# Optimization experiments

Hardware: AMD Instinct MI355X
Metric: run time of the kernel (lower is better)

## Reference

```python
import jax, jax.numpy as jnp
import numpy as np

N_NODES = 100000
IN_DIM = 128
HID_DIM = 128
N_EDGES = 1600000


def setup_inputs() -> dict:
    key = jax.random.key(0)
    k1, k2, k3, k4 = jax.random.split(key, 4)
    x = jax.random.normal(k1, (N_NODES, IN_DIM), dtype=jnp.float32)
    edge_index = jax.random.randint(k2, (2, N_EDGES), 0, N_NODES, dtype=jnp.int64)
    # GCNConv params (PyG: Linear(in, out, bias=False) + separate bias)
    scale = 1.0 / np.sqrt(IN_DIM)
    weight = jax.random.uniform(k3, (IN_DIM, HID_DIM), jnp.float32, -scale, scale)
    bias = jax.random.uniform(k4, (HID_DIM,), jnp.float32, -scale, scale)
    return {"x": x, "edge_index": edge_index, "weight": weight, "bias": bias}


def _gcn_forward(x, edge_index, weight, bias):
    n = x.shape[0]
    h = x @ weight  # [N, H] linear transform first (PyG order)
    # add self-loops
    loops = jnp.arange(n, dtype=edge_index.dtype)
    src = jnp.concatenate([edge_index[0], loops])
    dst = jnp.concatenate([edge_index[1], loops])
    # symmetric normalization: deg computed on destination (col) per PyG gcn_norm
    ones = jnp.ones_like(dst, dtype=h.dtype)
    deg = jax.ops.segment_sum(ones, dst, num_segments=n)  # [N]
    dinv = jnp.where(deg > 0, jax.lax.rsqrt(deg), 0.0)
    norm = dinv[src] * dinv[dst]  # [E+N]
    # message passing: out[dst] += norm * h[src]
    msg = h[src] * norm[:, None]  # [E+N, H] irregular gather (memory-bound)
    out = jax.ops.segment_sum(msg, dst, num_segments=n)  # scatter-add
    return out + bias


def reference(x, edge_index, weight, bias):
    h = _gcn_forward(x, edge_index, weight, bias)
    return jax.nn.relu(h)  # encoder_type != 'gat' -> ReLU
```

## Files before the change

### kernel.cpp

```cpp
#include <hip/hip_runtime.h>
#include <hip/hip_bf16.h>

#define N_NODES 100000
#define IN_DIM 128
#define HID_DIM 128
#define N_EDGES 1600000
#define NBK 196
#define BCAP 10240
#define BK_EDGES 4096
#define NBIN 391
#define NGEMM 1563
#define G1 625
#define G2 (NGEMM - G1)
#define LDK 136

using half8 = __attribute__((ext_vector_type(8))) _Float16;
using half4 = __attribute__((ext_vector_type(4))) _Float16;
using f32x4 = __attribute__((ext_vector_type(4))) float;

__global__ void k_prep(int* __restrict__ gcur, const float* __restrict__ w,
                       _Float16* __restrict__ wt) {
    int i = blockIdx.x * 256 + threadIdx.x;
    if (i < NBK) gcur[i] = 0;
    if (i < IN_DIM * HID_DIM) {
        int k = i >> 7, c = i & 127;
        wt[c * 128 + k] = (_Float16)w[i];
    }
}

__device__ __forceinline__ void gemm_role(char* smem, int tid, int brow,
                                          const float* __restrict__ x,
                                          const _Float16* __restrict__ wt,
                                          _Float16* __restrict__ h) {
    _Float16* xs = (_Float16*)smem;
    _Float16* ws = (_Float16*)(smem + 17408);
    {
        int row = tid >> 2;
        int seg = (tid & 3) * 32;
        int grow = brow + row; if (grow > N_NODES - 1) grow = N_NODES - 1;
        const float4* p = reinterpret_cast<const float4*>(&x[(size_t)grow * IN_DIM + seg]);
#pragma unroll
        for (int i = 0; i < 8; ++i) {
            float4 v = p[i];
            half4 hv = {(_Float16)v.x, (_Float16)v.y, (_Float16)v.z, (_Float16)v.w};
            *reinterpret_cast<half4*>(&xs[row * LDK + seg + i * 4]) = hv;
        }
    }
    {
        int row = tid >> 1;
        int seg = (tid & 1) * 64;
        const half8* p = reinterpret_cast<const half8*>(&wt[row * 128 + seg]);
#pragma unroll
        for (int i = 0; i < 8; ++i)
            *reinterpret_cast<half8*>(&ws[row * LDK + seg + i * 8]) = p[i];
    }
    __syncthreads();

    const int lane = tid & 63;
    const int m0   = (tid >> 6) * 16;
    const int arow = m0 + (lane & 15);
    const int kgrp = (lane >> 4) * 8;
    f32x4 acc[8] = {};
#pragma unroll
    for (int k0 = 0; k0 < 128; k0 += 32) {
        half8 a = *reinterpret_cast<const half8*>(&xs[arow * LDK + k0 + kgrp]);
#pragma unroll
        for (int nb = 0; nb < 8; ++nb) {
            half8 b = *reinterpret_cast<const half8*>(
                &ws[(nb * 16 + (lane & 15)) * LDK + k0 + kgrp]);
            acc[nb] = __builtin_amdgcn_mfma_f32_16x16x32_f16(a, b, acc[nb], 0, 0, 0);
        }
    }
#pragma unroll
    for (int nb = 0; nb < 8; ++nb) {
#pragma unroll
        for (int r = 0; r < 4; ++r) {
            int node = brow + m0 + (lane >> 4) * 4 + r;
            int feat = nb * 16 + (lane & 15);
            if (node < N_NODES) h[(size_t)node * HID_DIM + feat] = (_Float16)acc[nb][r];
        }
    }
}

__global__ __launch_bounds__(256) void k_fat1(const int* __restrict__ ei,
                                              const float* __restrict__ x,
                                              const _Float16* __restrict__ wt,
                                              _Float16* __restrict__ h,
                                              int* __restrict__ gcur,
                                              uint2* __restrict__ bucket) {
    __shared__ __align__(16) char smem[52224];
    const int tid = threadIdx.x;

    if (blockIdx.x >= NBIN) {
        gemm_role(smem, tid, (blockIdx.x - NBIN) * 64, x, wt, h);
        return;
    }
    uint2* stage = (uint2*)smem;
    int* hist  = (int*)(smem + 32768);
    int* lbase = (int*)(smem + 33552);
    int* lcur  = (int*)(smem + 34336);
    int* s64   = (int*)(smem + 35120);
    for (int b = tid; b < NBK; b += 256) { hist[b] = 0; lcur[b] = 0; }
    if (tid < 64) {
        int v = ei[2 * tid + 1];
        int all0 = __all(v == 0);
        if (tid == 0) *s64 = all0;
    }
    __syncthreads();
    const int is64 = *s64;
    const int e0 = blockIdx.x * BK_EDGES;
    const int valid = min(BK_EDGES, N_EDGES - e0);

#pragma unroll
    for (int k = 0; k < 8; ++k) {
        int el = k * 512 + 2 * tid;
        if (el >= valid) break;
        int e = e0 + el;
        int s0, s1, d0, d1;
        if (is64) {
            int4 vs = reinterpret_cast<const int4*>(ei)[e >> 1];
            int4 vd = (reinterpret_cast<const int4*>(ei) + N_EDGES / 2)[e >> 1];
            s0 = vs.x; s1 = vs.z; d0 = vd.x; d1 = vd.z;
        } else {
            int2 vs = reinterpret_cast<const int2*>(ei)[e >> 1];
            int2 vd = reinterpret_cast<const int2*>(ei + N_EDGES)[e >> 1];
            s0 = vs.x; s1 = vs.y; d0 = vd.x; d1 = vd.y;
        }
        stage[el]     = make_uint2((unsigned)s0, (unsigned)d0);
        stage[el + 1] = make_uint2((unsigned)s1, (unsigned)d1);
        atomicAdd(&hist[d0 >> 9], 1);
        atomicAdd(&hist[d1 >> 9], 1);
    }
    __syncthreads();
    for (int b = tid; b < NBK; b += 256)
        if (hist[b] > 0) lbase[b] = atomicAdd(&gcur[b], hist[b]);
    __syncthreads();
    for (int i = tid; i < valid; i += 256) {
        uint2 v = stage[i];
        int b = v.y >> 9;
        int pos = lbase[b] + atomicAdd(&lcur[b], 1);
        if (pos < BCAP) bucket[(size_t)b * BCAP + pos] = v;
    }
}

__global__ __launch_bounds__(256) void k_fat2(const int* __restrict__ gcur,
                                              const uint2* __restrict__ bucket,
                                              int* __restrict__ cnt,
                                              float* __restrict__ dinv,
                                              int* __restrict__ row_start,
                                              int* __restrict__ csr_src,
                                              const float* __restrict__ x,
                                              const _Float16* __restrict__ wt,
                                              _Float16* __restrict__ h) {
    __shared__ __align__(16) char smem[52224];
    const int tid = threadIdx.x;

    if (blockIdx.x >= NBK) {
        gemm_role(smem, tid, (G1 + blockIdx.x - NBK) * 64, x, wt, h);
        return;
    }
    int* sizes = (int*)smem;
    int* ncnt  = (int*)(smem + 784);
    int* nloff = (int*)(smem + 2832);
    int* ncur  = (int*)(smem + 4880);
    int* wtot  = (int*)(smem + 6928);
    int* base_p = (int*)(smem + 6944);
    const int b = blockIdx.x;
    for (int i = tid; i < NBK; i += 256) sizes[i] = gcur[i];
    ncnt[tid] = 0; ncnt[tid + 256] = 0; ncur[tid] = 0; ncur[tid + 256] = 0;
    __syncthreads();
    const int sz = min(sizes[b], BCAP);
    if (tid < 64) {
        int part = 0;
        for (int i = tid; i < b; i += 64) part += sizes[i];
#pragma unroll
        for (int d = 32; d; d >>= 1) part += __shfl_xor(part, d);
        if (tid == 0) *base_p = part;
    }
    const int n0 = b * 512;
    const uint2* bk = bucket + (size_t)b * BCAP;
    for (int i = tid; i < sz; i += 256) atomicAdd(&ncnt[bk[i].y - n0], 1);
    __syncthreads();
    int c0 = ncnt[2 * tid], c1 = ncnt[2 * tid + 1];
    int pair = c0 + c1;
    int lane = tid & 63, wv = tid >> 6;
    int scan = pair;
#pragma unroll
    for (int d = 1; d < 64; d <<= 1) {
        int t = __shfl_up(scan, d);
        if (lane >= d) scan += t;
    }
    if (lane == 63) wtot[wv] = scan;
    int excl = scan - pair;
    __syncthreads();
#pragma unroll
    for (int i = 0; i < 4; ++i) if (i < wv) excl += wtot[i];
    nloff[2 * tid] = excl;
    nloff[2 * tid + 1] = excl + c0;
    __syncthreads();
    const int base = *base_p;
    for (int i = tid; i < 512; i += 256) {
        int node = n0 + i;
        if (node < N_NODES) {
            int c = ncnt[i];
            cnt[node] = c;
            dinv[node] = rsqrtf((float)(c + 1));
            row_start[node] = base + nloff[i];
        }
    }
    for (int i = tid; i < sz; i += 256) {
        uint2 v = bk[i];
        int li = v.y - n0;
        int pos = atomicAdd(&ncur[li], 1);
        csr_src[base + nloff[li] + pos] = (int)v.x;
    }
}

#define GSTEP(J, SE, DS) {                                                   \
    int s_ = __shfl(SE, hi | (J));                                           \
    float w_ = __shfl(DS, hi | (J));                                         \
    half8 v_ = *reinterpret_cast<const half8*>(hbase + (size_t)s_ * HID_DIM);\
    acc[0] = fmaf((float)v_[0], w_, acc[0]);                                 \
    acc[1] = fmaf((float)v_[1], w_, acc[1]);                                 \
    acc[2] = fmaf((float)v_[2], w_, acc[2]);                                 \
    acc[3] = fmaf((float)v_[3], w_, acc[3]);                                 \
    acc[4] = fmaf((float)v_[4], w_, acc[4]);                                 \
    acc[5] = fmaf((float)v_[5], w_, acc[5]);                                 \
    acc[6] = fmaf((float)v_[6], w_, acc[6]);                                 \
    acc[7] = fmaf((float)v_[7], w_, acc[7]); }
#define GGRP(B, SE, DS) \
    GSTEP(B + 0, SE, DS) GSTEP(B + 1, SE, DS) GSTEP(B + 2, SE, DS) \
    GSTEP(B + 3, SE, DS) GSTEP(B + 4, SE, DS) GSTEP(B + 5, SE, DS) \
    GSTEP(B + 6, SE, DS) GSTEP(B + 7, SE, DS)

__global__ __launch_bounds__(256) void k_gather(const _Float16* __restrict__ h,
                                                const int* __restrict__ csr_src,
                                                const int* __restrict__ row_start,
                                                const int* __restrict__ cnt,
                                                const float* __restrict__ dinv,
                                                const float* __restrict__ bias,
                                                float* __restrict__ out) {
    const int lane = threadIdx.x & 63;
    const int l4   = lane & 15;
    const int hi   = lane & 48;
    const int node = blockIdx.x * 16 + (threadIdx.x >> 6) * 4 + (lane >> 4);
    const int rs = row_start[node];
    const int n  = cnt[node];
    const float di = dinv[node];
    const int tq = n + 1;
    const _Float16* hbase = h + l4 * 8;

    float acc[8] = {};

    for (int c0 = 0; c0 < tq; c0 += 32) {
        int t0 = c0 + l4, t1 = t0 + 16;
        int se0 = node, se1 = node;
        float dw0 = 0.0f, dw1 = 0.0f;
        if (t0 < n)       { se0 = csr_src[rs + t0]; dw0 = dinv[se0]; }
        else if (t0 == n)   dw0 = di;
        if (t1 < n)       { se1 = csr_src[rs + t1]; dw1 = dinv[se1]; }
        else if (t1 == n)   dw1 = di;

        GGRP(0, se0, dw0)
        if (tq <= c0 + 8) continue;
        GGRP(8, se0, dw0)
        if (tq <= c0 + 16) continue;
        GGRP(0, se1, dw1)
        if (tq <= c0 + 24) continue;
        GGRP(8, se1, dw1)
    }

    float4 bv0 = *reinterpret_cast<const float4*>(&bias[l4 * 8]);
    float4 bv1 = *reinterpret_cast<const float4*>(&bias[l4 * 8 + 4]);
    float4 o0, o1;
    o0.x = fmaxf(fmaf(di, acc[0], bv0.x), 0.0f);
    o0.y = fmaxf(fmaf(di, acc[1], bv0.y), 0.0f);
    o0.z = fmaxf(fmaf(di, acc[2], bv0.z), 0.0f);
    o0.w = fmaxf(fmaf(di, acc[3], bv0.w), 0.0f);
    o1.x = fmaxf(fmaf(di, acc[4], bv1.x), 0.0f);
    o1.y = fmaxf(fmaf(di, acc[5], bv1.y), 0.0f);
    o1.z = fmaxf(fmaf(di, acc[6], bv1.z), 0.0f);
    o1.w = fmaxf(fmaf(di, acc[7], bv1.w), 0.0f);
    *reinterpret_cast<float4*>(&out[(size_t)node * HID_DIM + l4 * 8])     = o0;
    *reinterpret_cast<float4*>(&out[(size_t)node * HID_DIM + l4 * 8 + 4]) = o1;
}

extern "C" void kernel_launch(void* const* d_in, const int* in_sizes, int n_in,
                              void* d_out, int out_size, void* d_ws, size_t ws_size,
                              hipStream_t stream) {
    const float* x    = (const float*)d_in[0];
    const int*   ei   = (const int*)d_in[1];
    const float* w    = (const float*)d_in[2];
    const float* bias = (const float*)d_in[3];
    float* out = (float*)d_out;

    char* wsb = (char*)d_ws;
    _Float16* h      = (_Float16*)(wsb);
    int*   cnt       = (int*)(wsb + 25600000);
    float* dinv      = (float*)(wsb + 26000000);
    int*   row_start = (int*)(wsb + 26400000);
    int*   csr_src   = (int*)(wsb + 26800000);
    uint2* bucket    = (uint2*)(wsb + 33200000);
    _Float16* wt     = (_Float16*)(wsb + 49256320);
    int*   gcur      = (int*)(wsb + 49289088);

    k_prep  <<<64, 256, 0, stream>>>(gcur, w, wt);
    k_fat1  <<<NBIN + G1, 256, 0, stream>>>(ei, x, wt, h, gcur, bucket);
    k_fat2  <<<NBK + G2, 256, 0, stream>>>(gcur, bucket, cnt, dinv, row_start, csr_src, x, wt, h);
    k_gather<<<N_NODES / 16, 256, 0, stream>>>(h, csr_src, row_start, cnt, dinv, bias, out);
}
```

Measured before the change: 123.3 us.

## Slice h by feature groups and gather per slice for cache locality

The GEMM now writes h in a feature-sliced layout: 8 slices of 16 features for all nodes. The gather kernel is restructured so each block handles one slice for a chunk of 128 nodes, with 2 lanes per node each accumulating 8 features over a sequential edge loop. The aim is to make each slice's working set small enough to stay in L2 during the random gathers. In exchange, edge indices and dinv are reread once per slice, each gather access is smaller, and per-lane loops serialize over node degree.

```diff
diff --git a/kernel.cpp b/kernel.cpp
--- a/kernel.cpp
+++ b/kernel.cpp
@@ -13,6 +13,9 @@
 #define G1 625
 #define G2 (NGEMM - G1)
 #define LDK 136
+#define SLICE_ELEMS (N_NODES * 16)
+#define GCHUNK 128
+#define NCHUNK ((N_NODES + GCHUNK - 1) / GCHUNK)
 
 using half8 = __attribute__((ext_vector_type(8))) _Float16;
 using half4 = __attribute__((ext_vector_type(4))) _Float16;
@@ -76,8 +79,9 @@
 #pragma unroll
         for (int r = 0; r < 4; ++r) {
             int node = brow + m0 + (lane >> 4) * 4 + r;
-            int feat = nb * 16 + (lane & 15);
-            if (node < N_NODES) h[(size_t)node * HID_DIM + feat] = (_Float16)acc[nb][r];
+            if (node < N_NODES)
+                h[(size_t)nb * SLICE_ELEMS + (size_t)node * 16 + (lane & 15)] =
+                    (_Float16)acc[nb][r];
         }
     }
 }
@@ -216,23 +220,6 @@
     }
 }
 
-#define GSTEP(J, SE, DS) {                                                   \
-    int s_ = __shfl(SE, hi | (J));                                           \
-    float w_ = __shfl(DS, hi | (J));                                         \
-    half8 v_ = *reinterpret_cast<const half8*>(hbase + (size_t)s_ * HID_DIM);\
-    acc[0] = fmaf((float)v_[0], w_, acc[0]);                                 \
-    acc[1] = fmaf((float)v_[1], w_, acc[1]);                                 \
-    acc[2] = fmaf((float)v_[2], w_, acc[2]);                                 \
-    acc[3] = fmaf((float)v_[3], w_, acc[3]);                                 \
-    acc[4] = fmaf((float)v_[4], w_, acc[4]);                                 \
-    acc[5] = fmaf((float)v_[5], w_, acc[5]);                                 \
-    acc[6] = fmaf((float)v_[6], w_, acc[6]);                                 \
-    acc[7] = fmaf((float)v_[7], w_, acc[7]); }
-#define GGRP(B, SE, DS) \
-    GSTEP(B + 0, SE, DS) GSTEP(B + 1, SE, DS) GSTEP(B + 2, SE, DS) \
-    GSTEP(B + 3, SE, DS) GSTEP(B + 4, SE, DS) GSTEP(B + 5, SE, DS) \
-    GSTEP(B + 6, SE, DS) GSTEP(B + 7, SE, DS)
-
 __global__ __launch_bounds__(256) void k_gather(const _Float16* __restrict__ h,
                                                 const int* __restrict__ csr_src,
                                                 const int* __restrict__ row_start,
@@ -240,49 +227,59 @@
                                                 const float* __restrict__ dinv,
                                                 const float* __restrict__ bias,
                                                 float* __restrict__ out) {
-    const int lane = threadIdx.x & 63;
-    const int l4   = lane & 15;
-    const int hi   = lane & 48;
-    const int node = blockIdx.x * 16 + (threadIdx.x >> 6) * 4 + (lane >> 4);
-    const int rs = row_start[node];
-    const int n  = cnt[node];
-    const float di = dinv[node];
-    const int tq = n + 1;
-    const _Float16* hbase = h + l4 * 8;
-
-    float acc[8] = {};
-
-    for (int c0 = 0; c0 < tq; c0 += 32) {
-        int t0 = c0 + l4, t1 = t0 + 16;
-        int se0 = node, se1 = node;
-        float dw0 = 0.0f, dw1 = 0.0f;
-        if (t0 < n)       { se0 = csr_src[rs + t0]; dw0 = dinv[se0]; }
-        else if (t0 == n)   dw0 = di;
-        if (t1 < n)       { se1 = csr_src[rs + t1]; dw1 = dinv[se1]; }
-        else if (t1 == n)   dw1 = di;
-
-        GGRP(0, se0, dw0)
-        if (tq <= c0 + 8) continue;
-        GGRP(8, se0, dw0)
-        if (tq <= c0 + 16) continue;
-        GGRP(0, se1, dw1)
-        if (tq <= c0 + 24) continue;
-        GGRP(8, se1, dw1)
-    }
-
-    float4 bv0 = *reinterpret_cast<const float4*>(&bias[l4 * 8]);
-    float4 bv1 = *reinterpret_cast<const float4*>(&bias[l4 * 8 + 4]);
-    float4 o0, o1;
-    o0.x = fmaxf(fmaf(di, acc[0], bv0.x), 0.0f);
-    o0.y = fmaxf(fmaf(di, acc[1], bv0.y), 0.0f);
-    o0.z = fmaxf(fmaf(di, acc[2], bv0.z), 0.0f);
-    o0.w = fmaxf(fmaf(di, acc[3], bv0.w), 0.0f);
-    o1.x = fmaxf(fmaf(di, acc[4], bv1.x), 0.0f);
-    o1.y = fmaxf(fmaf(di, acc[5], bv1.y), 0.0f);
-    o1.z = fmaxf(fmaf(di, acc[6], bv1.z), 0.0f);
-    o1.w = fmaxf(fmaf(di, acc[7], bv1.w), 0.0f);
-    *reinterpret_cast<float4*>(&out[(size_t)node * HID_DIM + l4 * 8])     = o0;
-    *reinterpret_cast<float4*>(&out[(size_t)node * HID_DIM + l4 * 8 + 4]) = o1;
+    const int slice = blockIdx.x & 7;
+    const int chunk = blockIdx.x >> 3;
+    const int lane  = threadIdx.x & 63;
+    const int oct   = lane & 1;
+    const int node  = chunk * GCHUNK + (threadIdx.x >> 6) * 32 + (lane >> 1);
+    const bool ok = node < N_NODES;
+    const int nd  = ok ? node : N_NODES - 1;
+    const int rs  = row_start[nd];
+    const int n   = ok ? cnt[nd] : 0;
+    const float di = dinv[nd];
+    const _Float16* hS = h + (size_t)slice * SLICE_ELEMS + oct * 8;
+
+    float acc[8];
+    {
+        half8 v = *reinterpret_cast<const half8*>(hS + (size_t)nd * 16);
+#pragma unroll
+        for (int k = 0; k < 8; ++k) acc[k] = di * (float)v[k];
+    }
+    int j = 0;
+    for (; j + 2 <= n; j += 2) {
+        int s0 = csr_src[rs + j], s1 = csr_src[rs + j + 1];
+        float w0 = dinv[s0], w1 = dinv[s1];
+        half8 v0 = *reinterpret_cast<const half8*>(hS + (size_t)s0 * 16);
+        half8 v1 = *reinterpret_cast<const half8*>(hS + (size_t)s1 * 16);
+#pragma unroll
+        for (int k = 0; k < 8; ++k) acc[k] = fmaf((float)v0[k], w0, acc[k]);
+#pragma unroll
+        for (int k = 0; k < 8; ++k) acc[k] = fmaf((float)v1[k], w1, acc[k]);
+    }
+    if (j < n) {
+        int s0 = csr_src[rs + j];
+        float w0 = dinv[s0];
+        half8 v0 = *reinterpret_cast<const half8*>(hS + (size_t)s0 * 16);
+#pragma unroll
+        for (int k = 0; k < 8; ++k) acc[k] = fmaf((float)v0[k], w0, acc[k]);
+    }
+    if (ok) {
+        const int fb = slice * 16 + oct * 8;
+        float4 bv0 = *reinterpret_cast<const float4*>(&bias[fb]);
+        float4 bv1 = *reinterpret_cast<const float4*>(&bias[fb + 4]);
+        float4 o0, o1;
+        o0.x = fmaxf(fmaf(di, acc[0], bv0.x), 0.0f);
+        o0.y = fmaxf(fmaf(di, acc[1], bv0.y), 0.0f);
+        o0.z = fmaxf(fmaf(di, acc[2], bv0.z), 0.0f);
+        o0.w = fmaxf(fmaf(di, acc[3], bv0.w), 0.0f);
+        o1.x = fmaxf(fmaf(di, acc[4], bv1.x), 0.0f);
+        o1.y = fmaxf(fmaf(di, acc[5], bv1.y), 0.0f);
+        o1.z = fmaxf(fmaf(di, acc[6], bv1.z), 0.0f);
+        o1.w = fmaxf(fmaf(di, acc[7], bv1.w), 0.0f);
+        float* op = &out[(size_t)node * HID_DIM + fb];
+        *reinterpret_cast<float4*>(op)     = o0;
+        *reinterpret_cast<float4*>(op + 4) = o1;
+    }
 }
 
 extern "C" void kernel_launch(void* const* d_in, const int* in_sizes, int n_in,
@@ -307,5 +304,5 @@
     k_prep  <<<64, 256, 0, stream>>>(gcur, w, wt);
     k_fat1  <<<NBIN + G1, 256, 0, stream>>>(ei, x, wt, h, gcur, bucket);
     k_fat2  <<<NBK + G2, 256, 0, stream>>>(gcur, bucket, cnt, dinv, row_start, csr_src, x, wt, h);
-    k_gather<<<N_NODES / 16, 256, 0, stream>>>(h, csr_src, row_start, cnt, dinv, bias, out);
-}
+    k_gather<<<NCHUNK * 8, 256, 0, stream>>>(h, csr_src, row_start, cnt, dinv, bias, out);
+}
```

New measurement: 219.4 us. 77.9% more time.

## Pack bucket entries into 32-bit words and merge row_start/count arrays

Applied to the files above, without the earlier changes.

Bucket entries are now stored as one 32-bit word (source shifted left by 9, plus the local destination index), with the bucket id kept separately in shared memory. This halves bucket write and read traffic and shrinks shared staging. k_fat2 holds up to 40 entries per thread in registers so the bucket is read once instead of twice. row_start and cnt are merged into one int2 array so the gather kernel does a single load per node. The costs are higher register pressure in k_fat2 and reliance on source ids fitting in 23 bits.

```diff
diff --git a/kernel.cpp b/kernel.cpp
--- a/kernel.cpp
+++ b/kernel.cpp
@@ -87,7 +87,7 @@
                                               const _Float16* __restrict__ wt,
                                               _Float16* __restrict__ h,
                                               int* __restrict__ gcur,
-                                              uint2* __restrict__ bucket) {
+                                              unsigned* __restrict__ bucket) {
     __shared__ __align__(16) char smem[52224];
     const int tid = threadIdx.x;
 
@@ -95,11 +95,12 @@
         gemm_role(smem, tid, (blockIdx.x - NBIN) * 64, x, wt, h);
         return;
     }
-    uint2* stage = (uint2*)smem;
-    int* hist  = (int*)(smem + 32768);
-    int* lbase = (int*)(smem + 33552);
-    int* lcur  = (int*)(smem + 34336);
-    int* s64   = (int*)(smem + 35120);
+    unsigned* stage = (unsigned*)smem;
+    unsigned char* bkid = (unsigned char*)(smem + 16384);
+    int* hist  = (int*)(smem + 20480);
+    int* lbase = (int*)(smem + 21264);
+    int* lcur  = (int*)(smem + 22048);
+    int* s64   = (int*)(smem + 22832);
     for (int b = tid; b < NBK; b += 256) { hist[b] = 0; lcur[b] = 0; }
     if (tid < 64) {
         int v = ei[2 * tid + 1];
@@ -126,8 +127,10 @@
             int2 vd = reinterpret_cast<const int2*>(ei + N_EDGES)[e >> 1];
             s0 = vs.x; s1 = vs.y; d0 = vd.x; d1 = vd.y;
         }
-        stage[el]     = make_uint2((unsigned)s0, (unsigned)d0);
-        stage[el + 1] = make_uint2((unsigned)s1, (unsigned)d1);
+        stage[el]     = ((unsigned)s0 << 9) | ((unsigned)d0 & 511u);
+        stage[el + 1] = ((unsigned)s1 << 9) | ((unsigned)d1 & 511u);
+        bkid[el]      = (unsigned char)(d0 >> 9);
+        bkid[el + 1]  = (unsigned char)(d1 >> 9);
         atomicAdd(&hist[d0 >> 9], 1);
         atomicAdd(&hist[d1 >> 9], 1);
     }
@@ -136,18 +139,17 @@
         if (hist[b] > 0) lbase[b] = atomicAdd(&gcur[b], hist[b]);
     __syncthreads();
     for (int i = tid; i < valid; i += 256) {
-        uint2 v = stage[i];
-        int b = v.y >> 9;
+        unsigned v = stage[i];
+        int b = bkid[i];
         int pos = lbase[b] + atomicAdd(&lcur[b], 1);
         if (pos < BCAP) bucket[(size_t)b * BCAP + pos] = v;
     }
 }
 
 __global__ __launch_bounds__(256) void k_fat2(const int* __restrict__ gcur,
-                                              const uint2* __restrict__ bucket,
-                                              int* __restrict__ cnt,
+                                              const unsigned* __restrict__ bucket,
                                               float* __restrict__ dinv,
-                                              int* __restrict__ row_start,
+                                              int2* __restrict__ rc,
                                               int* __restrict__ csr_src,
                                               const float* __restrict__ x,
                                               const _Float16* __restrict__ wt,
@@ -178,8 +180,15 @@
         if (tid == 0) *base_p = part;
     }
     const int n0 = b * 512;
-    const uint2* bk = bucket + (size_t)b * BCAP;
-    for (int i = tid; i < sz; i += 256) atomicAdd(&ncnt[bk[i].y - n0], 1);
+    const unsigned* bk = bucket + (size_t)b * BCAP;
+    unsigned ent[40];
+#pragma unroll
+    for (int j = 0; j < 40; ++j) {
+        int i = j * 256 + tid;
+        unsigned v = 0xFFFFFFFFu;
+        if (i < sz) { v = bk[i]; atomicAdd(&ncnt[v & 511u], 1); }
+        ent[j] = v;
+    }
     __syncthreads();
     int c0 = ncnt[2 * tid], c1 = ncnt[2 * tid + 1];
     int pair = c0 + c1;
@@ -203,16 +212,18 @@
         int node = n0 + i;
         if (node < N_NODES) {
             int c = ncnt[i];
-            cnt[node] = c;
             dinv[node] = rsqrtf((float)(c + 1));
-            row_start[node] = base + nloff[i];
-        }
-    }
-    for (int i = tid; i < sz; i += 256) {
-        uint2 v = bk[i];
-        int li = v.y - n0;
-        int pos = atomicAdd(&ncur[li], 1);
-        csr_src[base + nloff[li] + pos] = (int)v.x;
+            rc[node] = make_int2(base + nloff[i], c);
+        }
+    }
+#pragma unroll
+    for (int j = 0; j < 40; ++j) {
+        unsigned v = ent[j];
+        if (v != 0xFFFFFFFFu) {
+            int li = v & 511u;
+            int pos = atomicAdd(&ncur[li], 1);
+            csr_src[base + nloff[li] + pos] = (int)(v >> 9);
+        }
     }
 }
 
@@ -235,8 +246,7 @@
 
 __global__ __launch_bounds__(256) void k_gather(const _Float16* __restrict__ h,
                                                 const int* __restrict__ csr_src,
-                                                const int* __restrict__ row_start,
-                                                const int* __restrict__ cnt,
+                                                const int2* __restrict__ rc,
                                                 const float* __restrict__ dinv,
                                                 const float* __restrict__ bias,
                                                 float* __restrict__ out) {
@@ -244,8 +254,9 @@
     const int l4   = lane & 15;
     const int hi   = lane & 48;
     const int node = blockIdx.x * 16 + (threadIdx.x >> 6) * 4 + (lane >> 4);
-    const int rs = row_start[node];
-    const int n  = cnt[node];
+    const int2 rcv = rc[node];
+    const int rs = rcv.x;
+    const int n  = rcv.y;
     const float di = dinv[node];
     const int tq = n + 1;
     const _Float16* hbase = h + l4 * 8;
@@ -281,8 +292,9 @@
     o1.y = fmaxf(fmaf(di, acc[5], bv1.y), 0.0f);
     o1.z = fmaxf(fmaf(di, acc[6], bv1.z), 0.0f);
     o1.w = fmaxf(fmaf(di, acc[7], bv1.w), 0.0f);
-    *reinterpret_cast<float4*>(&out[(size_t)node * HID_DIM + l4 * 8])     = o0;
-    *reinterpret_cast<float4*>(&out[(size_t)node * HID_DIM + l4 * 8 + 4]) = o1;
+    float* op = &out[(size_t)node * HID_DIM + l4 * 8];
+    *reinterpret_cast<float4*>(op)     = o0;
+    *reinterpret_cast<float4*>(op + 4) = o1;
 }
 
 extern "C" void kernel_launch(void* const* d_in, const int* in_sizes, int n_in,
@@ -296,16 +308,15 @@
 
     char* wsb = (char*)d_ws;
     _Float16* h      = (_Float16*)(wsb);
-    int*   cnt       = (int*)(wsb + 25600000);
-    float* dinv      = (float*)(wsb + 26000000);
-    int*   row_start = (int*)(wsb + 26400000);
+    float* dinv      = (float*)(wsb + 25600000);
+    int2*  rc        = (int2*)(wsb + 26000000);
     int*   csr_src   = (int*)(wsb + 26800000);
-    uint2* bucket    = (uint2*)(wsb + 33200000);
-    _Float16* wt     = (_Float16*)(wsb + 49256320);
-    int*   gcur      = (int*)(wsb + 49289088);
+    unsigned* bucket = (unsigned*)(wsb + 33200000);
+    _Float16* wt     = (_Float16*)(wsb + 41228160);
+    int*   gcur      = (int*)(wsb + 41260928);
 
     k_prep  <<<64, 256, 0, stream>>>(gcur, w, wt);
     k_fat1  <<<NBIN + G1, 256, 0, stream>>>(ei, x, wt, h, gcur, bucket);
-    k_fat2  <<<NBK + G2, 256, 0, stream>>>(gcur, bucket, cnt, dinv, row_start, csr_src, x, wt, h);
-    k_gather<<<N_NODES / 16, 256, 0, stream>>>(h, csr_src, row_start, cnt, dinv, bias, out);
-}
+    k_fat2  <<<NBK + G2, 256, 0, stream>>>(gcur, bucket, dinv, rc, csr_src, x, wt, h);
+    k_gather<<<N_NODES / 16, 256, 0, stream>>>(h, csr_src, rc, dinv, bias, out);
+}
```

Measured after the change: 120.6 us. 1.02x faster.
